# Performance work log

Hardware: AMD Instinct MI355X
Metric: run time of the kernel (lower is better)

The kernel has to match this reference:

```python
import jax, jax.numpy as jnp
import numpy as np

B, T = 65536, 200
H, S, P = 512, 1000, 5
EPS = 1e-6


def setup_inputs() -> dict:
    key = jax.random.key(0)
    ks = jax.random.split(key, 8)
    init = lambda k, shp, fan: (jax.random.normal(k, shp, jnp.float32) / np.float32(np.sqrt(fan)))
    return {
        "X": jax.random.randint(ks[0], (B,), 0, S, dtype=jnp.int32),
        "y": jax.random.randint(ks[1], (B, T), 0, 2, dtype=jnp.int32),
        "embed": init(ks[2], (S, H), 1.0),
        "W1": init(ks[3], (H, H), H), "b1": jnp.zeros((H,), jnp.float32),
        "W2": init(ks[4], (H, H), H), "b2": jnp.zeros((H,), jnp.float32),
        "Wout": init(ks[5], (H, P), H), "bout": jnp.zeros((P,), jnp.float32),
    }


def reference(X, y, embed, W1, b1, W2, b2, Wout, bout):
    # --- MLP over skill embeddings: params (B, 5) = (l, f, g, s, latent0) ---
    e = embed[X]                                    # (B, H)
    h = jax.nn.relu(e @ W1 + b1)                    # num_layers = 2
    h = jax.nn.relu(h @ W2 + b2)
    params = jnp.clip(jax.nn.sigmoid(h @ Wout + bout), EPS, 1.0 - EPS)  # (B, 5)
    l, g, s = params[:, 0], params[:, 2], params[:, 3]
    latent0 = params[:, 4]                          # (B,)

    y_clean = jnp.where(y == -1, 0, y).astype(jnp.float32)  # (B, T)

    # --- BKT latent-update recurrence over T steps ---
    def step(latent, y_t):
        num1 = latent * (1.0 - s)
        correct = num1 + (1.0 - latent) * g
        k_t1 = num1 / correct
        k_t0 = latent * s / (latent * s + (1.0 - latent) * (1.0 - g))
        k_t = jnp.where(y_t > 0.5, k_t1, k_t0)
        nxt = jnp.clip(k_t + (1.0 - k_t) * l, EPS, 1.0 - EPS)
        return nxt, (correct, latent)

    _, (corrects, latents) = jax.lax.scan(step, latent0, y_clean.T)  # (T, B) each
    return corrects.T, latents.T, params
```

## Files before the change

kernel.cpp:

```cpp
#include <hip/hip_runtime.h>


typedef unsigned int uint;
typedef unsigned char uchar;
typedef unsigned short ushort_t;
typedef __attribute__((ext_vector_type(8))) short short8;
typedef __attribute__((ext_vector_type(4))) float f32x4;

#define SS 1000
#define HH 512
#define TT 200
#define BB_ 65536
#define PP 5

#define OFF_EMB   0
#define OFF_B1    512000
#define OFF_B2    512512
#define OFF_WOUT  513024
#define OFF_BOUT  515584
#define CONV_TOT  515589

__device__ __forceinline__ float b2f(ushort_t u) {
    return __uint_as_float(((uint)u) << 16);
}
__device__ __forceinline__ ushort_t f2b(float f) {
    uint u = __float_as_uint(f);
    uint r = u + 0x7FFFu + ((u >> 16) & 1u);
    return (ushort_t)(r >> 16);
}
__device__ __forceinline__ int detect_bf16(const uint* __restrict__ embed_raw,
                                           int tid) {
    uint w = embed_raw[tid & 63];
    uint e = (w >> 7) & 0xFFu;
    bool pl = (e >= 117u && e <= 130u);
    return __popcll(__ballot(pl)) >= 32 ? 1 : 0;
}
__device__ __forceinline__ ushort_t ld_bf16(const void* src, int idx, int fb) {
    return fb ? ((const ushort_t*)src)[idx] : f2b(((const float*)src)[idx]);
}

__global__ __launch_bounds__(256) void prep_kernel(
    const void* __restrict__ embed, const void* __restrict__ W1,
    const void* __restrict__ b1,    const void* __restrict__ W2,
    const void* __restrict__ b2,    const void* __restrict__ Wout,
    const void* __restrict__ bout,
    ushort_t* __restrict__ conv, ushort_t* __restrict__ WT1,
    ushort_t* __restrict__ WT2)
{
    int tid = threadIdx.x;
    int fb = detect_bf16((const uint*)embed, tid);
    int bx = blockIdx.x;
    if (bx < 2015) {
        int i = bx * 256 + tid;
        if (i < CONV_TOT) {
            const void* src; int off;
            if      (i < OFF_B1)   { src = embed; off = i; }
            else if (i < OFF_B2)   { src = b1;    off = i - OFF_B1; }
            else if (i < OFF_WOUT) { src = b2;    off = i - OFF_B2; }
            else if (i < OFF_BOUT) { src = Wout;  off = i - OFF_WOUT; }
            else                   { src = bout;  off = i - OFF_BOUT; }
            conv[i] = ld_bf16(src, off, fb);
        }
    } else {
        __shared__ ushort_t t[32][33];
        int bi = bx - 2015;
        const void* W = bi < 256 ? W1 : W2;
        ushort_t* WT = bi < 256 ? WT1 : WT2;
        int ti = bi & 255;
        int k0 = (ti & 15) * 32, n0 = (ti >> 4) * 32;
        int tx = tid & 31, ty = tid >> 5;
        #pragma unroll
        for (int i = ty; i < 32; i += 8)
            t[i][tx] = ld_bf16(W, (k0 + i) * HH + n0 + tx, fb);
        __syncthreads();
        #pragma unroll
        for (int i = ty; i < 32; i += 8)
            WT[(n0 + i) * HH + k0 + tx] = t[tx][i];
    }
}

__global__ __launch_bounds__(256) void mlp_layer(
    const ushort_t* __restrict__ A, const ushort_t* __restrict__ WT,
    const ushort_t* __restrict__ bias, ushort_t* __restrict__ H, int Mclamp)
{
    int tid = threadIdx.x;
    int lane = tid & 63;
    int wave = tid >> 6;
    int m_base = blockIdx.x * 64 + wave * 16;
    int n_base = blockIdx.y * 64;
    int lrow = lane & 15;
    int q = lane >> 4;
    int rowA = m_base + lrow; if (rowA > Mclamp) rowA = Mclamp;

    const short8* Ap  = (const short8*)(A + (size_t)rowA * HH) + q;
    const short8* Bp0 = (const short8*)(WT + (size_t)(n_base + 0 * 16 + lrow) * HH) + q;
    const short8* Bp1 = (const short8*)(WT + (size_t)(n_base + 1 * 16 + lrow) * HH) + q;
    const short8* Bp2 = (const short8*)(WT + (size_t)(n_base + 2 * 16 + lrow) * HH) + q;
    const short8* Bp3 = (const short8*)(WT + (size_t)(n_base + 3 * 16 + lrow) * HH) + q;

    f32x4 acc0 = {0.f,0.f,0.f,0.f}, acc1 = {0.f,0.f,0.f,0.f};
    f32x4 acc2 = {0.f,0.f,0.f,0.f}, acc3 = {0.f,0.f,0.f,0.f};

    #pragma unroll 4
    for (int kk = 0; kk < 16; kk++) {
        short8 a   = Ap[kk * 4];
        short8 b0  = Bp0[kk * 4];
        short8 b1v = Bp1[kk * 4];
        short8 b2v = Bp2[kk * 4];
        short8 b3v = Bp3[kk * 4];
        acc0 = __builtin_amdgcn_mfma_f32_16x16x32_bf16(a, b0,  acc0, 0, 0, 0);
        acc1 = __builtin_amdgcn_mfma_f32_16x16x32_bf16(a, b1v, acc1, 0, 0, 0);
        acc2 = __builtin_amdgcn_mfma_f32_16x16x32_bf16(a, b2v, acc2, 0, 0, 0);
        acc3 = __builtin_amdgcn_mfma_f32_16x16x32_bf16(a, b3v, acc3, 0, 0, 0);
    }

    int orow = m_base + q * 4;
    f32x4 accs[4] = {acc0, acc1, acc2, acc3};
    #pragma unroll
    for (int nt = 0; nt < 4; nt++) {
        int n = n_base + nt * 16 + lrow;
        float bb = b2f(bias[n]);
        #pragma unroll
        for (int r = 0; r < 4; r++) {
            float v = accs[nt][r] + bb;
            H[(size_t)(orow + r) * HH + n] = f2b(fmaxf(v, 0.f));
        }
    }
}

__global__ __launch_bounds__(256) void params_kernel(
    const ushort_t* __restrict__ h2, const ushort_t* __restrict__ conv,
    float* __restrict__ table)
{
    int wid = blockIdx.x * 4 + (threadIdx.x >> 6);
    int lane = threadIdx.x & 63;
    if (wid >= SS * PP) return;
    int row = wid / PP, p = wid - row * PP;
    const ushort_t* Wout = conv + OFF_WOUT;
    const ushort_t* bout = conv + OFF_BOUT;
    const short8* hr = (const short8*)(h2 + (size_t)row * HH);
    short8 h = hr[lane];
    float acc = 0.f;
    #pragma unroll
    for (int j = 0; j < 8; j++) {
        int k = lane * 8 + j;
        acc += b2f((ushort_t)h[j]) * b2f(Wout[k * PP + p]);
    }
    #pragma unroll
    for (int m = 32; m; m >>= 1) acc += __shfl_xor(acc, m);
    if (lane == 0) {
        float x = acc + b2f(bout[p]);
        float sg = 1.f / (1.f + expf(-x));
        sg = fminf(fmaxf(sg, 1e-6f), 1.f - 1e-6f);
        table[(size_t)row * 8 + p] = sg;
    }
}

__global__ __launch_bounds__(64) void scan_kernel(
    const int* __restrict__ X, const int* __restrict__ y,
    const float* __restrict__ table, const uint* __restrict__ embed_raw,
    void* __restrict__ out)
{
    __shared__ uchar yb[64 * 52];
    __shared__ __align__(16) uint stg[2][64 * 42];
    int tid = threadIdx.x;
    int b0 = blockIdx.x * 64;
    int b = b0 + tid;
    int fb = detect_bf16(embed_raw, tid);

    #pragma unroll
    for (int k2 = 0; k2 < 50; k2++) {
        int gix = tid + k2 * 64;
        int r = gix / 50, q = gix - r * 50;
        int4 v = *(const int4*)(y + (size_t)(b0 + r) * TT + q * 4);
        yb[r * 52 + q] = (uchar)((uint)(v.x == 1) | ((uint)(v.y == 1) << 1) |
                                 ((uint)(v.z == 1) << 2) | ((uint)(v.w == 1) << 3));
    }

    int xi = X[b]; xi = xi < 0 ? 0 : (xi >= SS ? SS - 1 : xi);
    float l      = table[xi * 8 + 0];
    float p1     = table[xi * 8 + 1];
    float g      = table[xi * 8 + 2];
    float s      = table[xi * 8 + 3];
    float latent = table[xi * 8 + 4];

    if (fb) {
        ushort_t* pout = (ushort_t*)out + 2ull * BB_ * TT + (size_t)b * 5;
        pout[0] = f2b(l); pout[1] = f2b(p1); pout[2] = f2b(g);
        pout[3] = f2b(s); pout[4] = f2b(latent);
    } else {
        float* pout = (float*)out + 2ull * BB_ * TT + (size_t)b * 5;
        pout[0] = l; pout[1] = p1; pout[2] = g; pout[3] = s; pout[4] = latent;
    }

    char* cgb = (char*)out;
    char* lgb = (char*)out + (fb ? 2ull : 4ull) * BB_ * TT;
    float oms = 1.f - s;
    float omg = 1.f - g;
    float A1  = 1.f - s - g;
    float A0  = s + g - 1.f;
    float oml = 1.f - l;

    __syncthreads();

    for (int c = 0; c < 5; c++) {
        #pragma unroll
        for (int j4 = 0; j4 < 10; j4++) {
            uint u = yb[tid * 52 + c * 10 + j4];
            uint pc0 = 0, pc1 = 0, pl0 = 0, pl1 = 0;
            #pragma unroll
            for (int i = 0; i < 4; i++) {
                float num1    = latent * oms;
                float correct = fmaf(latent, A1, g);
                float lats    = latent * s;
                bool yt = (u >> i) & 1u;
                float num = yt ? num1 : lats;
                float den = yt ? correct : fmaf(latent, A0, omg);
                float kt  = num * __builtin_amdgcn_rcpf(den);
                if (!fb) {
                    stg[0][tid * 42 + j4 * 4 + i] = __float_as_uint(correct);
                    stg[1][tid * 42 + j4 * 4 + i] = __float_as_uint(latent);
                } else {
                    uint cb = (uint)f2b(correct), lb = (uint)f2b(latent);
                    if (i == 0)      { pc0 = cb;        pl0 = lb; }
                    else if (i == 1) { pc0 |= cb << 16; pl0 |= lb << 16; }
                    else if (i == 2) { pc1 = cb;        pl1 = lb; }
                    else             { pc1 |= cb << 16; pl1 |= lb << 16; }
                }
                float nxt = fmaf(kt, oml, l);
                latent = fminf(fmaxf(nxt, 1e-6f), 1.f - 1e-6f);
            }
            if (fb) {
                stg[0][tid * 21 + j4 * 2]     = pc0;
                stg[0][tid * 21 + j4 * 2 + 1] = pc1;
                stg[1][tid * 21 + j4 * 2]     = pl0;
                stg[1][tid * 21 + j4 * 2 + 1] = pl1;
            }
        }
        __syncthreads();
        if (!fb) {
            #pragma unroll
            for (int k2 = 0; k2 < 20; k2++) {
                int gix = tid + k2 * 64;
                int r = gix / 20, q = gix - r * 20;
                uint2 vc = *(const uint2*)&stg[0][r * 42 + q * 2];
                uint2 vl = *(const uint2*)&stg[1][r * 42 + q * 2];
                size_t off = (size_t)(b0 + r) * 800 + (size_t)c * 160 + q * 8;
                *(uint2*)(cgb + off) = vc;
                *(uint2*)(lgb + off) = vl;
            }
        } else {
            #pragma unroll
            for (int k2 = 0; k2 < 10; k2++) {
                int gix = tid + k2 * 64;
                int r = gix / 10, q = gix - r * 10;
                size_t off = (size_t)(b0 + r) * 400 + (size_t)c * 80 + q * 4;
                *(uint*)(cgb + off) = stg[0][r * 21 + q];
                *(uint*)(lgb + off) = stg[1][r * 21 + q];
            }
        }
        __syncthreads();
    }
}

extern "C" void kernel_launch(void* const* d_in, const int* in_sizes, int n_in,
                              void* d_out, int out_size, void* d_ws, size_t ws_size,
                              hipStream_t stream) {
    const int* X = (const int*)d_in[0];
    const int* y = (const int*)d_in[1];

    char* ws = (char*)d_ws;
    ushort_t* conv  = (ushort_t*)(ws);
    ushort_t* WT1   = (ushort_t*)(ws + 1048576);
    ushort_t* WT2   = (ushort_t*)(ws + 1572864);
    ushort_t* h1    = (ushort_t*)(ws + 2097152);
    ushort_t* h2    = (ushort_t*)(ws + 3145728);
    float*    table = (float*)(ws + 4194304);

    prep_kernel<<<dim3(2527, 1, 1), 256, 0, stream>>>(
        d_in[2], d_in[3], d_in[4], d_in[5], d_in[6], d_in[7], d_in[8],
        conv, WT1, WT2);
    mlp_layer<<<dim3(16, 8, 1), 256, 0, stream>>>(conv + OFF_EMB, WT1, conv + OFF_B1, h1, SS - 1);
    mlp_layer<<<dim3(16, 8, 1), 256, 0, stream>>>(h1, WT2, conv + OFF_B2, h2, 1023);
    params_kernel<<<dim3(1250, 1, 1), 256, 0, stream>>>(h2, conv, table);
    scan_kernel<<<dim3(BB_ / 64, 1, 1), 64, 0, stream>>>(
        X, y, table, (const uint*)d_in[2], (void*)d_out);
}
```

Baseline: 218.7 us.

## Split BKT scan into checkpoint pass and parallel segment replay; shrink MLP N-tile

The single scan kernel is replaced by two passes. The first runs the recurrence per row without storing outputs, saving the latent value and packed y bits at each of 8 segment boundaries of 25 steps. The second launches 8 threads per row, and each replays its own segment and writes correct and latent directly to global memory. This raises parallelism for the output-writing phase and drops the shared-memory staging, at the cost of computing the recurrence twice and writing outputs uncoalesced (each thread writes contiguous elements, while neighbouring threads sit 25 elements apart). The MLP layer tile is also reduced from 64 to 16 output columns per block, giving more blocks but less reuse of the A operand.

```diff
diff --git a/kernel.cpp b/kernel.cpp
--- a/kernel.cpp
+++ b/kernel.cpp
@@ -2,7 +2,6 @@
 
 
 typedef unsigned int uint;
-typedef unsigned char uchar;
 typedef unsigned short ushort_t;
 typedef __attribute__((ext_vector_type(8))) short short8;
 typedef __attribute__((ext_vector_type(4))) float f32x4;
@@ -37,6 +36,22 @@
 }
 __device__ __forceinline__ ushort_t ld_bf16(const void* src, int idx, int fb) {
     return fb ? ((const ushort_t*)src)[idx] : f2b(((const float*)src)[idx]);
+}
+
+__device__ __forceinline__ float bkt_step(float latent, bool yt,
+                                          float oms, float omg, float A1,
+                                          float A0, float g, float s,
+                                          float oml, float l,
+                                          float* correct_out) {
+    float num1    = latent * oms;
+    float correct = fmaf(latent, A1, g);
+    float lats    = latent * s;
+    float num = yt ? num1 : lats;
+    float den = yt ? correct : fmaf(latent, A0, omg);
+    float kt  = num * __builtin_amdgcn_rcpf(den);
+    *correct_out = correct;
+    float nxt = fmaf(kt, oml, l);
+    return fminf(fmaxf(nxt, 1e-6f), 1.f - 1e-6f);
 }
 
 __global__ __launch_bounds__(256) void prep_kernel(
@@ -87,44 +102,29 @@
     int lane = tid & 63;
     int wave = tid >> 6;
     int m_base = blockIdx.x * 64 + wave * 16;
-    int n_base = blockIdx.y * 64;
+    int n_base = blockIdx.y * 16;
     int lrow = lane & 15;
     int q = lane >> 4;
     int rowA = m_base + lrow; if (rowA > Mclamp) rowA = Mclamp;
 
-    const short8* Ap  = (const short8*)(A + (size_t)rowA * HH) + q;
-    const short8* Bp0 = (const short8*)(WT + (size_t)(n_base + 0 * 16 + lrow) * HH) + q;
-    const short8* Bp1 = (const short8*)(WT + (size_t)(n_base + 1 * 16 + lrow) * HH) + q;
-    const short8* Bp2 = (const short8*)(WT + (size_t)(n_base + 2 * 16 + lrow) * HH) + q;
-    const short8* Bp3 = (const short8*)(WT + (size_t)(n_base + 3 * 16 + lrow) * HH) + q;
-
-    f32x4 acc0 = {0.f,0.f,0.f,0.f}, acc1 = {0.f,0.f,0.f,0.f};
-    f32x4 acc2 = {0.f,0.f,0.f,0.f}, acc3 = {0.f,0.f,0.f,0.f};
-
-    #pragma unroll 4
+    const short8* Ap = (const short8*)(A + (size_t)rowA * HH) + q;
+    const short8* Bp = (const short8*)(WT + (size_t)(n_base + lrow) * HH) + q;
+
+    f32x4 acc = {0.f, 0.f, 0.f, 0.f};
+    #pragma unroll 8
     for (int kk = 0; kk < 16; kk++) {
-        short8 a   = Ap[kk * 4];
-        short8 b0  = Bp0[kk * 4];
-        short8 b1v = Bp1[kk * 4];
-        short8 b2v = Bp2[kk * 4];
-        short8 b3v = Bp3[kk * 4];
-        acc0 = __builtin_amdgcn_mfma_f32_16x16x32_bf16(a, b0,  acc0, 0, 0, 0);
-        acc1 = __builtin_amdgcn_mfma_f32_16x16x32_bf16(a, b1v, acc1, 0, 0, 0);
-        acc2 = __builtin_amdgcn_mfma_f32_16x16x32_bf16(a, b2v, acc2, 0, 0, 0);
-        acc3 = __builtin_amdgcn_mfma_f32_16x16x32_bf16(a, b3v, acc3, 0, 0, 0);
+        short8 a = Ap[kk * 4];
+        short8 b = Bp[kk * 4];
+        acc = __builtin_amdgcn_mfma_f32_16x16x32_bf16(a, b, acc, 0, 0, 0);
     }
 
     int orow = m_base + q * 4;
-    f32x4 accs[4] = {acc0, acc1, acc2, acc3};
-    #pragma unroll
-    for (int nt = 0; nt < 4; nt++) {
-        int n = n_base + nt * 16 + lrow;
-        float bb = b2f(bias[n]);
-        #pragma unroll
-        for (int r = 0; r < 4; r++) {
-            float v = accs[nt][r] + bb;
-            H[(size_t)(orow + r) * HH + n] = f2b(fmaxf(v, 0.f));
-        }
+    int n = n_base + lrow;
+    float bb = b2f(bias[n]);
+    #pragma unroll
+    for (int r = 0; r < 4; r++) {
+        float v = acc[r] + bb;
+        H[(size_t)(orow + r) * HH + n] = f2b(fmaxf(v, 0.f));
     }
 }
 
@@ -156,110 +156,96 @@
     }
 }
 
-__global__ __launch_bounds__(64) void scan_kernel(
+__global__ __launch_bounds__(256) void scan_a(
     const int* __restrict__ X, const int* __restrict__ y,
-    const float* __restrict__ table, const uint* __restrict__ embed_raw,
-    void* __restrict__ out)
-{
-    __shared__ uchar yb[64 * 52];
-    __shared__ __align__(16) uint stg[2][64 * 42];
-    int tid = threadIdx.x;
-    int b0 = blockIdx.x * 64;
-    int b = b0 + tid;
-    int fb = detect_bf16(embed_raw, tid);
-
-    #pragma unroll
-    for (int k2 = 0; k2 < 50; k2++) {
-        int gix = tid + k2 * 64;
-        int r = gix / 50, q = gix - r * 50;
-        int4 v = *(const int4*)(y + (size_t)(b0 + r) * TT + q * 4);
-        yb[r * 52 + q] = (uchar)((uint)(v.x == 1) | ((uint)(v.y == 1) << 1) |
-                                 ((uint)(v.z == 1) << 2) | ((uint)(v.w == 1) << 3));
-    }
-
-    int xi = X[b]; xi = xi < 0 ? 0 : (xi >= SS ? SS - 1 : xi);
+    const float* __restrict__ table,
+    float* __restrict__ cpA, uint* __restrict__ maskA)
+{
+    int r = blockIdx.x * 256 + threadIdx.x;
+    const int4* yrow = (const int4*)(y + (size_t)r * TT);
+    uint u[8] = {0, 0, 0, 0, 0, 0, 0, 0};
+    #pragma unroll
+    for (int k = 0; k < 50; k++) {
+        int4 v = yrow[k];
+        int t = 4 * k;
+        u[(t + 0) / 25] |= (uint)(v.x == 1) << ((t + 0) % 25);
+        u[(t + 1) / 25] |= (uint)(v.y == 1) << ((t + 1) % 25);
+        u[(t + 2) / 25] |= (uint)(v.z == 1) << ((t + 2) % 25);
+        u[(t + 3) / 25] |= (uint)(v.w == 1) << ((t + 3) % 25);
+    }
+
+    int xi = X[r]; xi = xi < 0 ? 0 : (xi >= SS ? SS - 1 : xi);
     float l      = table[xi * 8 + 0];
-    float p1     = table[xi * 8 + 1];
     float g      = table[xi * 8 + 2];
     float s      = table[xi * 8 + 3];
     float latent = table[xi * 8 + 4];
-
-    if (fb) {
-        ushort_t* pout = (ushort_t*)out + 2ull * BB_ * TT + (size_t)b * 5;
-        pout[0] = f2b(l); pout[1] = f2b(p1); pout[2] = f2b(g);
-        pout[3] = f2b(s); pout[4] = f2b(latent);
-    } else {
-        float* pout = (float*)out + 2ull * BB_ * TT + (size_t)b * 5;
-        pout[0] = l; pout[1] = p1; pout[2] = g; pout[3] = s; pout[4] = latent;
-    }
+    float oms = 1.f - s, omg = 1.f - g, oml = 1.f - l;
+    float A1 = 1.f - s - g, A0 = s + g - 1.f;
+
+    float cp[8];
+    #pragma unroll
+    for (int w = 0; w < 8; w++) {
+        cp[w] = latent;
+        uint uw = u[w];
+        #pragma unroll
+        for (int i = 0; i < 25; i++) {
+            float cdummy;
+            latent = bkt_step(latent, (uw >> i) & 1u,
+                              oms, omg, A1, A0, g, s, oml, l, &cdummy);
+        }
+    }
+    #pragma unroll
+    for (int w = 0; w < 8; w++) {
+        cpA[(size_t)w * BB_ + r]   = cp[w];
+        maskA[(size_t)w * BB_ + r] = u[w];
+    }
+}
+
+__global__ __launch_bounds__(256) void scan_b(
+    const int* __restrict__ X, const float* __restrict__ table,
+    const float* __restrict__ cpA, const uint* __restrict__ maskA,
+    const uint* __restrict__ embed_raw, void* __restrict__ out)
+{
+    int tid = blockIdx.x * 256 + threadIdx.x;
+    int r = tid >> 3;
+    int j = tid & 7;
+    int fb = detect_bf16(embed_raw, threadIdx.x);
+
+    int xi = X[r]; xi = xi < 0 ? 0 : (xi >= SS ? SS - 1 : xi);
+    float l  = table[xi * 8 + 0];
+    float p1 = table[xi * 8 + 1];
+    float g  = table[xi * 8 + 2];
+    float s  = table[xi * 8 + 3];
+    float L0 = table[xi * 8 + 4];
+
+    if (j < 5) {
+        float pv = j == 0 ? l : j == 1 ? p1 : j == 2 ? g : j == 3 ? s : L0;
+        size_t po = 2ull * BB_ * TT + (size_t)r * 5 + j;
+        if (fb) ((ushort_t*)out)[po] = f2b(pv);
+        else    ((float*)out)[po] = pv;
+    }
+
+    float latent = cpA[(size_t)j * BB_ + r];
+    uint  u      = maskA[(size_t)j * BB_ + r];
+    float oms = 1.f - s, omg = 1.f - g, oml = 1.f - l;
+    float A1 = 1.f - s - g, A0 = s + g - 1.f;
 
     char* cgb = (char*)out;
     char* lgb = (char*)out + (fb ? 2ull : 4ull) * BB_ * TT;
-    float oms = 1.f - s;
-    float omg = 1.f - g;
-    float A1  = 1.f - s - g;
-    float A0  = s + g - 1.f;
-    float oml = 1.f - l;
-
-    __syncthreads();
-
-    for (int c = 0; c < 5; c++) {
-        #pragma unroll
-        for (int j4 = 0; j4 < 10; j4++) {
-            uint u = yb[tid * 52 + c * 10 + j4];
-            uint pc0 = 0, pc1 = 0, pl0 = 0, pl1 = 0;
-            #pragma unroll
-            for (int i = 0; i < 4; i++) {
-                float num1    = latent * oms;
-                float correct = fmaf(latent, A1, g);
-                float lats    = latent * s;
-                bool yt = (u >> i) & 1u;
-                float num = yt ? num1 : lats;
-                float den = yt ? correct : fmaf(latent, A0, omg);
-                float kt  = num * __builtin_amdgcn_rcpf(den);
-                if (!fb) {
-                    stg[0][tid * 42 + j4 * 4 + i] = __float_as_uint(correct);
-                    stg[1][tid * 42 + j4 * 4 + i] = __float_as_uint(latent);
-                } else {
-                    uint cb = (uint)f2b(correct), lb = (uint)f2b(latent);
-                    if (i == 0)      { pc0 = cb;        pl0 = lb; }
-                    else if (i == 1) { pc0 |= cb << 16; pl0 |= lb << 16; }
-                    else if (i == 2) { pc1 = cb;        pl1 = lb; }
-                    else             { pc1 |= cb << 16; pl1 |= lb << 16; }
-                }
-                float nxt = fmaf(kt, oml, l);
-                latent = fminf(fmaxf(nxt, 1e-6f), 1.f - 1e-6f);
-            }
-            if (fb) {
-                stg[0][tid * 21 + j4 * 2]     = pc0;
-                stg[0][tid * 21 + j4 * 2 + 1] = pc1;
-                stg[1][tid * 21 + j4 * 2]     = pl0;
-                stg[1][tid * 21 + j4 * 2 + 1] = pl1;
-            }
+    size_t eoff = (size_t)r * TT + j * 25;
+    #pragma unroll
+    for (int i = 0; i < 25; i++) {
+        float correct;
+        float nxt = bkt_step(latent, (u >> i) & 1u,
+                             oms, omg, A1, A0, g, s, oml, l, &correct);
+        if (fb) {
+            ((ushort_t*)cgb)[eoff + i] = f2b(correct);
+            ((ushort_t*)lgb)[eoff + i] = f2b(latent);
+        } else {
+            ((float*)cgb)[eoff + i] = correct;
+            ((float*)lgb)[eoff + i] = latent;
         }
-        __syncthreads();
-        if (!fb) {
-            #pragma unroll
-            for (int k2 = 0; k2 < 20; k2++) {
-                int gix = tid + k2 * 64;
-                int r = gix / 20, q = gix - r * 20;
-                uint2 vc = *(const uint2*)&stg[0][r * 42 + q * 2];
-                uint2 vl = *(const uint2*)&stg[1][r * 42 + q * 2];
-                size_t off = (size_t)(b0 + r) * 800 + (size_t)c * 160 + q * 8;
-                *(uint2*)(cgb + off) = vc;
-                *(uint2*)(lgb + off) = vl;
-            }
-        } else {
-            #pragma unroll
-            for (int k2 = 0; k2 < 10; k2++) {
-                int gix = tid + k2 * 64;
-                int r = gix / 10, q = gix - r * 10;
-                size_t off = (size_t)(b0 + r) * 400 + (size_t)c * 80 + q * 4;
-                *(uint*)(cgb + off) = stg[0][r * 21 + q];
-                *(uint*)(lgb + off) = stg[1][r * 21 + q];
-            }
-        }
-        __syncthreads();
+        latent = nxt;
     }
 }
 
@@ -276,13 +262,16 @@
     ushort_t* h1    = (ushort_t*)(ws + 2097152);
     ushort_t* h2    = (ushort_t*)(ws + 3145728);
     float*    table = (float*)(ws + 4194304);
+    float*    cpA   = (float*)(ws + 4227072);
+    uint*     maskA = (uint*)(ws + 6324224);
 
     prep_kernel<<<dim3(2527, 1, 1), 256, 0, stream>>>(
         d_in[2], d_in[3], d_in[4], d_in[5], d_in[6], d_in[7], d_in[8],
         conv, WT1, WT2);
-    mlp_layer<<<dim3(16, 8, 1), 256, 0, stream>>>(conv + OFF_EMB, WT1, conv + OFF_B1, h1, SS - 1);
-    mlp_layer<<<dim3(16, 8, 1), 256, 0, stream>>>(h1, WT2, conv + OFF_B2, h2, 1023);
+    mlp_layer<<<dim3(16, 32, 1), 256, 0, stream>>>(conv + OFF_EMB, WT1, conv + OFF_B1, h1, SS - 1);
+    mlp_layer<<<dim3(16, 32, 1), 256, 0, stream>>>(h1, WT2, conv + OFF_B2, h2, 1023);
     params_kernel<<<dim3(1250, 1, 1), 256, 0, stream>>>(h2, conv, table);
-    scan_kernel<<<dim3(BB_ / 64, 1, 1), 64, 0, stream>>>(
-        X, y, table, (const uint*)d_in[2], (void*)d_out);
-}
+    scan_a<<<dim3(BB_ / 256, 1, 1), 256, 0, stream>>>(X, y, table, cpA, maskA);
+    scan_b<<<dim3((BB_ * 8) / 256, 1, 1), 256, 0, stream>>>(
+        X, table, cpA, maskA, (const uint*)d_in[2], (void*)d_out);
+}
```

Result: slower. 346.7 us (+58.5%).
